# Kernel tuning notes

Hardware: AMD Instinct MI355X
Metric: run time of the kernel (lower is better)

## Reference

```python
import jax, jax.numpy as jnp
import numpy as np

N, D, GN, UVW = 64, 32, 128, 64
EMB = H = 256
NONSP, SPA = 8, 2
ACT = NONSP + 4          # 12
GOA = 256 + ACT          # fc3 + action = 268
GLO = H + GOA            # 524
SW = 64


def _conv3(x, w, b):
    # 3x3, stride 1, pad 1, NCHW / OIHW (torch layout)
    y = jax.lax.conv_general_dilated(x, w, (1, 1), ((1, 1), (1, 1)),
                                     dimension_numbers=('NCHW', 'OIHW', 'NCHW'))
    return y + b[None, :, None, None]


def _up2(x):
    # bilinear x2, half-pixel centers (matches torch align_corners=False)
    n, c, h, w = x.shape
    return jax.image.resize(x, (n, c, 2 * h, 2 * w), 'bilinear')


def setup_inputs() -> dict:
    key = jax.random.key(0)
    ks = jax.random.split(key, 24)
    def rn(k, shape, s=0.05):
        return jax.random.normal(k, shape, jnp.float32) * s
    G = (jax.random.uniform(ks[0], (N, D, GN, GN)) < 0.1).astype(jnp.float32)
    avail = jax.random.randint(ks[2], (N, NONSP), 0, 2).astype(jnp.int32)
    avail = avail.at[:, 0].set(1)  # guarantee at least one available action
    return {
        'G': G,
        'X': rn(ks[1], (N, D, GN, UVW), 1.0),
        'avail_actions': avail,
        'LSTM_hidden': jnp.zeros((2, 1, N, H), jnp.float32),
        'prev_actions': rn(ks[3], (N, D, ACT), 1.0),
        'relevant_frames': jax.random.randint(ks[4], (N, D), 0, 2).astype(jnp.int32),
        'We': rn(ks[5], (UVW, EMB)), 'be': jnp.zeros((EMB,)),
        'W1': rn(ks[6], (EMB, 256)), 'b1': jnp.zeros((256,)),
        'W2': rn(ks[7], (256, 256)), 'b2': jnp.zeros((256,)),
        'W3': rn(ks[8], (256, 256)), 'b3': jnp.zeros((256,)),
        'Wle': rn(ks[9], (GOA, H)), 'ble': jnp.zeros((H,)),
        'Wih': rn(ks[10], (4 * H, H)), 'Whh': rn(ks[11], (4 * H, H)),
        'bih': jnp.zeros((4 * H,)), 'bhh': jnp.zeros((4 * H,)),
        'Wa': rn(ks[12], (GLO, NONSP)), 'ba': jnp.zeros((NONSP,)),
        'Wv': rn(ks[13], (GLO, 1)), 'bv': jnp.zeros((1,)),
        'Wt1': rn(ks[14], (GLO, 256, 4, 4)), 'bt1': jnp.zeros((256,)),
        'Wc2': rn(ks[15], (128, 256, 3, 3)), 'bc2': jnp.zeros((128,)),
        'Wc3': rn(ks[16], (64, 128, 3, 3)), 'bc3': jnp.zeros((64,)),
        'Wc4': rn(ks[17], (64, 64, 3, 3)), 'bc4': jnp.zeros((64,)),
        'Wc5': rn(ks[18], (64, 64, 3, 3)), 'bc5': jnp.zeros((64,)),
        'Wc6': rn(ks[19], (SPA, 64, 3, 3)), 'bc6': jnp.zeros((SPA,)),
    }


def reference(G, X, avail_actions, LSTM_hidden, prev_actions, relevant_frames,
              We, be, W1, b1, W2, b2, W3, b3, Wle, ble, Wih, Whh, bih, bhh,
              Wa, ba, Wv, bv, Wt1, bt1, Wc2, bc2, Wc3, bc3, Wc4, bc4,
              Wc5, bc5, Wc6, bc6):
    n = G.shape[0]
    eye = jnp.eye(GN, dtype=G.dtype)

    def step(carry, xs):
        h, c, _, _ = carry
        Gc, Xc, pa, rel = xs            # [n,GN,GN], [n,GN,UVW], [n,ACT], [n]
        A = Gc + eye
        dis = 1.0 / jnp.sqrt(jnp.maximum(A.sum(-1), 1.0))
        A_agg = A * dis[:, :, None] * dis[:, None, :]  # D^-1/2 A D^-1/2
        emb = jnp.tanh(Xc @ We + be)
        h1 = jnp.tanh(A_agg @ (emb @ W1 + b1))
        h2 = jnp.tanh(A_agg @ (h1 @ W2 + b2))
        h3 = jnp.tanh(A_agg @ (h2 @ W3 + b3))
        goa = jnp.concatenate([h3.max(axis=1), pa], axis=1)  # [n, GOA]
        xin = jnp.tanh(goa @ Wle + ble)
        gates = xin @ Wih.T + bih + h @ Whh.T + bhh
        i, f, g, o = jnp.split(gates, 4, axis=1)
        c_new = jax.nn.sigmoid(f) * c + jax.nn.sigmoid(i) * jnp.tanh(g)
        h_new = jax.nn.sigmoid(o) * jnp.tanh(c_new)
        keep = (rel != 0).astype(h_new.dtype)[:, None]  # reset hidden for irrelevant frames
        return (h_new * keep, c_new * keep, h_new, goa), None

    h0, c0 = LSTM_hidden[0, 0], LSTM_hidden[1, 0]
    goa0 = jnp.zeros((n, GOA), G.dtype)
    xs = (jnp.swapaxes(G, 0, 1), jnp.swapaxes(X, 0, 1),
          jnp.swapaxes(prev_actions, 0, 1), jnp.swapaxes(relevant_frames, 0, 1))
    (hf, cf, hout, goa), _ = jax.lax.scan(step, (h0, c0, h0, goa0), xs)

    glo = jnp.concatenate([hout, goa], axis=1)  # [n, 524]
    logits = glo @ Wa + ba
    logits = jnp.where(avail_actions == 0, -jnp.inf, logits)
    nonspatial_policy = jax.nn.softmax(logits, axis=1)
    value = glo @ Wv + bv

    # deconv on 1x1 input == einsum with torch [in,out,kh,kw] weight
    s1 = jax.nn.leaky_relu(jnp.einsum('nc,cfhw->nfhw', glo, Wt1) + bt1[None, :, None, None], 0.1)
    # note: original F.relu(x, 0.1) is plain relu (0.1 lands in `inplace`)
    s2 = jax.nn.relu(_up2(_conv3(s1, Wc2, bc2)))
    s3 = jax.nn.relu(_up2(_conv3(s2, Wc3, bc3)))
    s4 = jax.nn.relu(_up2(_conv3(s3, Wc4, bc4)))
    s5 = jax.nn.relu(_up2(_conv3(s4, Wc5, bc5)))
    sl = _conv3(s5, Wc6, bc6).reshape(n, SPA, -1)
    spatial_policy = jax.nn.softmax(sl, axis=2).reshape(n, SPA, SW, SW)

    LSTM_hidden_out = jnp.stack([hf, cf])[:, None]  # [2,1,n,H]
    return (spatial_policy, nonspatial_policy, value, LSTM_hidden_out)
```

## Files before the change

### kernel.cpp

```cpp
#include <hip/hip_runtime.h>
#include <math.h>

typedef unsigned short u16;
typedef unsigned int u32;

typedef __attribute__((ext_vector_type(8))) short bf16x8;
typedef __attribute__((ext_vector_type(4))) float f32x4;

__device__ __forceinline__ float b2f(u16 u) {
    union { u32 ui; float f; } v; v.ui = ((u32)u) << 16; return v.f;
}
__device__ __forceinline__ float b2f_lo(u32 u) {
    union { u32 ui; float f; } v; v.ui = u << 16; return v.f;
}
__device__ __forceinline__ float b2f_hi(u32 u) {
    union { u32 ui; float f; } v; v.ui = u & 0xffff0000u; return v.f;
}
__device__ __forceinline__ u16 f2b(float f) {
    union { float f; u32 ui; } v; v.f = f;
    u32 x = v.ui;
    u32 r = (x + 0x7fffu + ((x >> 16) & 1u)) >> 16;
    return (u16)r;
}
__device__ __forceinline__ float sigf(float x) { return 1.0f / (1.0f + expf(-x)); }
__device__ __forceinline__ float ftanh(float x) {
    float e = __expf(2.0f * x);
    return 1.0f - 2.0f / (e + 1.0f);
}

#define GNODES 128
#define EMBD   256
#define NB     64
#define TS     32
#define GOA    268
#define GLO    524

#define OUT_SPATIAL 0
#define OUT_NS      524288
#define OUT_V       524800
#define OUT_H       524864

#define WS_GOA   ((size_t)0)
#define WS_HBUF  ((size_t)2195456)
#define WS_CBUF  ((size_t)2260992)
#define WS_HOUT  ((size_t)2326528)
#define WS_GLO   ((size_t)2392064)
#define WS_WIHT  ((size_t)2526208)
#define WS_WHHT  ((size_t)3574784)
#define WS_BSUM  ((size_t)4623360)
#define WS_C2    ((size_t)4627456)
#define WS_C3    ((size_t)4889600)
#define WS_C4    ((size_t)5413888)
#define WS_C5    ((size_t)7511040)
#define WS_SL    ((size_t)15899648)
#define WS_WET   ((size_t)16948224)
#define WS_W1T   ((size_t)16980992)
#define WS_W2T   ((size_t)17112064)
#define WS_W3T   ((size_t)17243136)
#define WS_GX    ((size_t)17374208)
#define WS_S1F   ((size_t)25762816)

#define WS_WP4   WS_GOA
#define WS_WP5   (WS_GOA + (size_t)196608)
#define WS_WP3   (WS_GOA + (size_t)393216)
#define WS_WP2   WS_GX

#define SA_S 264
#define TT_S 136
#define XS_S 72

__global__ void wprep(const float* __restrict__ We, const float* __restrict__ W1,
                      const float* __restrict__ W2, const float* __restrict__ W3,
                      u16* __restrict__ WeT, u16* __restrict__ W1T,
                      u16* __restrict__ W2T, u16* __restrict__ W3T)
{
    int idx = blockIdx.x * 256 + threadIdx.x;
    if (idx < 16384) {
        int k = idx >> 8, nn = idx & 255;
        WeT[nn * 64 + k] = f2b(We[idx]);
    }
    {
        int k = idx >> 8, nn = idx & 255;
        W1T[nn * 256 + k] = f2b(W1[idx]);
        W2T[nn * 256 + k] = f2b(W2[idx]);
        W3T[nn * 256 + k] = f2b(W3[idx]);
    }
}

__global__ __launch_bounds__(1024, 4) void gcn_mfma(
    const float* __restrict__ G, const float* __restrict__ X, const float* __restrict__ pa,
    const u16* __restrict__ WeT, const float* __restrict__ be,
    const u16* __restrict__ W1T, const float* __restrict__ b1,
    const u16* __restrict__ W2T, const float* __restrict__ b2,
    const u16* __restrict__ W3T, const float* __restrict__ b3,
    float* __restrict__ goaAll)
{
    __shared__ u16 Sa[128 * SA_S];
    __shared__ u16 Tt[256 * TT_S];
    __shared__ float dis[GNODES];
    __shared__ float dred[1024];
    __shared__ float pm[256];

    const int item = blockIdx.x;
    const int tid  = threadIdx.x;
    const int wv   = tid >> 6;
    const int nt   = wv & 7;
    const int ch   = wv >> 3;
    const int lane = tid & 63;
    const int l16  = lane & 15;
    const int quad = lane >> 4;
    const float* Gp = G + (size_t)item * GNODES * GNODES;
    const float* Xp = X + (size_t)item * GNODES * 64;

    for (int idx = tid; idx < 128 * 64; idx += 1024) {
        int m = idx >> 6, k = idx & 63;
        Tt[m * XS_S + k] = f2b(Xp[idx]);
    }
    {
        int row = tid >> 3, part = tid & 7;
        const float4* gr = (const float4*)(Gp + (size_t)row * GNODES) + part * 4;
        float s = 0.f;
#pragma unroll
        for (int k = 0; k < 4; ++k) { float4 g = gr[k]; s += g.x + g.y + g.z + g.w; }
        dred[tid] = s;
    }
    __syncthreads();
    if (tid < GNODES) {
        float s = 0.f;
#pragma unroll
        for (int p = 0; p < 8; ++p) s += dred[tid * 8 + p];
        dis[tid] = 1.0f / sqrtf(s + 1.0f);
    }
    __syncthreads();

    bf16x8 bAgg[4];
    {
        const int i = nt * 16 + l16;
        const float di = dis[i];
        const float* gr = Gp + (size_t)i * GNODES;
#pragma unroll
        for (int t = 0; t < 4; ++t) {
            const int k0 = t * 32 + quad * 8;
            float4 ga = *(const float4*)(gr + k0);
            float4 gb = *(const float4*)(gr + k0 + 4);
            float vv[8] = {ga.x, ga.y, ga.z, ga.w, gb.x, gb.y, gb.z, gb.w};
            bf16x8 f;
#pragma unroll
            for (int j = 0; j < 8; ++j) {
                int k = k0 + j;
                float a = (vv[j] + (k == i ? 1.0f : 0.0f)) * di * dis[k];
                f[j] = (short)f2b(a);
            }
            bAgg[t] = f;
        }
    }

    {
        bf16x8 a0 = *(const bf16x8*)(Tt + (16 * nt + l16) * XS_S + quad * 8);
        bf16x8 a1 = *(const bf16x8*)(Tt + (16 * nt + l16) * XS_S + 32 + quad * 8);
        for (int cj = 0; cj < 8; ++cj) {
            const int ct = ch * 8 + cj;
            const int nf = ct * 16 + l16;
            bf16x8 wb0 = *(const bf16x8*)(WeT + nf * 64 + quad * 8);
            bf16x8 wb1 = *(const bf16x8*)(WeT + nf * 64 + 32 + quad * 8);
            float bb = be[nf];
            f32x4 acc = {bb, bb, bb, bb};
            acc = __builtin_amdgcn_mfma_f32_16x16x32_bf16(a0, wb0, acc, 0, 0, 0);
            acc = __builtin_amdgcn_mfma_f32_16x16x32_bf16(a1, wb1, acc, 0, 0, 0);
#pragma unroll
            for (int r = 0; r < 4; ++r) {
                int node = 16 * nt + quad * 4 + r;
                Sa[node * SA_S + nf] = f2b(ftanh(acc[r]));
            }
        }
    }
    __syncthreads();

    const u16* WTs[3]  = {W1T, W2T, W3T};
    const float* bss[3] = {b1, b2, b3};

    for (int l = 0; l < 3; ++l) {
        const u16* WT = WTs[l];
        const float* bias = bss[l];

        const int nf = wv * 16 + l16;
        const float bb = bias[nf];
        bf16x8 bfr[8];
#pragma unroll
        for (int t = 0; t < 8; ++t)
            bfr[t] = *(const bf16x8*)(WT + (size_t)nf * 256 + t * 32 + quad * 8);

        for (int rt = 0; rt < 8; ++rt) {
            bf16x8 afr[8];
#pragma unroll
            for (int t = 0; t < 8; ++t)
                afr[t] = *(const bf16x8*)(Sa + (16 * rt + l16) * SA_S + t * 32 + quad * 8);
            f32x4 acc = {bb, bb, bb, bb};
#pragma unroll
            for (int t = 0; t < 8; ++t)
                acc = __builtin_amdgcn_mfma_f32_16x16x32_bf16(afr[t], bfr[t], acc, 0, 0, 0);
            u16 p0 = f2b(acc[0]), p1 = f2b(acc[1]), p2 = f2b(acc[2]), p3 = f2b(acc[3]);
            uint2 pk; pk.x = (u32)p0 | ((u32)p1 << 16); pk.y = (u32)p2 | ((u32)p3 << 16);
            *(uint2*)(Tt + (size_t)nf * TT_S + 16 * rt + quad * 4) = pk;
        }
        __syncthreads();

        for (int fj = 0; fj < 8; ++fj) {
            const int ft = ch * 8 + fj;
            bf16x8 afr[4];
#pragma unroll
            for (int t = 0; t < 4; ++t)
                afr[t] = *(const bf16x8*)(Tt + (16 * ft + l16) * TT_S + t * 32 + quad * 8);
            f32x4 acc = {0.f, 0.f, 0.f, 0.f};
#pragma unroll
            for (int t = 0; t < 4; ++t)
                acc = __builtin_amdgcn_mfma_f32_16x16x32_bf16(afr[t], bAgg[t], acc, 0, 0, 0);
            int i = nt * 16 + l16;
            u16 p0 = f2b(ftanh(acc[0])), p1 = f2b(ftanh(acc[1]));
            u16 p2 = f2b(ftanh(acc[2])), p3 = f2b(ftanh(acc[3]));
            uint2 pk; pk.x = (u32)p0 | ((u32)p1 << 16); pk.y = (u32)p2 | ((u32)p3 << 16);
            *(uint2*)(Sa + (size_t)i * SA_S + 16 * ft + quad * 4) = pk;
        }
        __syncthreads();
    }

    const int nb = item >> 5, tt = item & 31;
    float* gdst = goaAll + ((size_t)tt * NB + nb) * GOA;
    float mymax = -2.0f;
    if (tid < 512) {
        int f = tid & 255, h = tid >> 8;
        for (int i = h * 64; i < h * 64 + 64; ++i)
            mymax = fmaxf(mymax, b2f(Sa[i * SA_S + f]));
        if (h == 1) pm[f] = mymax;
    }
    __syncthreads();
    if (tid < 256) {
        gdst[tid] = fmaxf(mymax, pm[tid]);
    } else if (tid >= 512 && tid < 524) {
        gdst[256 + (tid - 512)] = pa[(size_t)item * 12 + (tid - 512)];
    }
}

__global__ void wtrans(const float* __restrict__ Wih, const float* __restrict__ Whh,
                       const float* __restrict__ bih, const float* __restrict__ bhh,
                       float* __restrict__ wihT, float* __restrict__ whhT, float* __restrict__ bsum)
{
    int idx = blockIdx.x * 256 + threadIdx.x;
    int r = idx >> 8;
    int k = idx & 255;
    wihT[k * 1024 + r] = Wih[idx];
    whhT[k * 1024 + r] = Whh[idx];
    if (idx < 1024) bsum[idx] = bih[idx] + bhh[idx];
}

#define LP_IT 8
__global__ __launch_bounds__(256) void lstm_pre(
    const float* __restrict__ goaAll, const float* __restrict__ Wle, const float* __restrict__ ble,
    const float* __restrict__ wihT, const float* __restrict__ bsum,
    float* __restrict__ gatesX)
{
    __shared__ float gl[LP_IT][GOA];
    __shared__ float xv[LP_IT][256];
    const int b0 = blockIdx.x * LP_IT;
    const int u = threadIdx.x;

    for (int idx = u; idx < LP_IT * GOA; idx += 256) {
        int it = idx / GOA, k = idx - it * GOA;
        gl[it][k] = goaAll[(size_t)(b0 + it) * GOA + k];
    }
    __syncthreads();

    {
        float acc[LP_IT];
        float bl = ble[u];
#pragma unroll
        for (int i = 0; i < LP_IT; ++i) acc[i] = bl;
        for (int k = 0; k < GOA; ++k) {
            float w = Wle[k * 256 + u];
#pragma unroll
            for (int i = 0; i < LP_IT; ++i) acc[i] = fmaf(gl[i][k], w, acc[i]);
        }
#pragma unroll
        for (int i = 0; i < LP_IT; ++i) xv[i][u] = tanhf(acc[i]);
    }
    __syncthreads();

#pragma unroll
    for (int g = 0; g < 4; ++g) {
        float a[LP_IT];
        float bs = bsum[g * 256 + u];
#pragma unroll
        for (int i = 0; i < LP_IT; ++i) a[i] = bs;
#pragma unroll 4
        for (int k = 0; k < 256; ++k) {
            float w = wihT[k * 1024 + g * 256 + u];
#pragma unroll
            for (int i = 0; i < LP_IT; ++i) a[i] = fmaf(xv[i][k], w, a[i]);
        }
#pragma unroll
        for (int i = 0; i < LP_IT; ++i)
            gatesX[(size_t)(b0 + i) * 1024 + g * 256 + u] = a[i];
    }
}

__global__ __launch_bounds__(1024) void lstm_seq(
    const float* __restrict__ gatesX, const float* __restrict__ whhT,
    const int* __restrict__ relf, const float* __restrict__ lh,
    float* __restrict__ hbuf, float* __restrict__ cbuf, float* __restrict__ hout)
{
    __shared__ float hv[256];
    __shared__ float ga[1024];
    __shared__ int hzf;
    const int n = blockIdx.x, u = threadIdx.x;
    float cpriv = 0.f;
    if (u < 256) { hv[u] = lh[n * 256 + u]; cpriv = lh[16384 + n * 256 + u]; }
    if (u == 0) hzf = 0;
    __syncthreads();

    for (int t = 0; t < TS; ++t) {
        float a = gatesX[((size_t)t * NB + n) * 1024 + u];
        if (!hzf) {
            const float* wh = whhT + u;
            float a0 = 0.f, a1 = 0.f, a2 = 0.f, a3 = 0.f;
#pragma unroll 4
            for (int k = 0; k < 256; k += 4) {
                a0 = fmaf(hv[k],     wh[(k)     * 1024], a0);
                a1 = fmaf(hv[k + 1], wh[(k + 1) * 1024], a1);
                a2 = fmaf(hv[k + 2], wh[(k + 2) * 1024], a2);
                a3 = fmaf(hv[k + 3], wh[(k + 3) * 1024], a3);
            }
            a += (a0 + a1) + (a2 + a3);
        }
        ga[u] = a;
        __syncthreads();
        if (u < 256) {
            float ai = ga[u], af = ga[256 + u], ag = ga[512 + u], ao = ga[768 + u];
            float cn = sigf(af) * cpriv + sigf(ai) * tanhf(ag);
            float hn = sigf(ao) * tanhf(cn);
            float kp = (relf[n * TS + t] != 0) ? 1.f : 0.f;
            if (t == TS - 1) {
                hout[n * 256 + u] = hn;
                hbuf[n * 256 + u] = hn * kp;
                cbuf[n * 256 + u] = cn * kp;
            }
            cpriv = cn * kp;
            hv[u] = hn * kp;
        }
        if (u == 0) hzf = (relf[n * TS + t] != 0) ? 0 : 1;
        __syncthreads();
    }
}

__global__ __launch_bounds__(256) void heads(
    const float* __restrict__ goaAll, const float* __restrict__ hout,
    const float* __restrict__ hbuf, const float* __restrict__ cbuf,
    const float* __restrict__ Wa, const float* __restrict__ ba,
    const float* __restrict__ Wv, const float* __restrict__ bv,
    const int* __restrict__ avail, float* __restrict__ glo, float* __restrict__ out)
{
    __shared__ float gl[GLO];
    __shared__ float lg[8];
    const int n = blockIdx.x, tid = threadIdx.x;
    const float* gsrc = goaAll + ((size_t)31 * NB + n) * GOA;
    gl[tid] = hout[n * 256 + tid];
    gl[256 + tid] = gsrc[tid];
    if (tid < 12) gl[512 + tid] = gsrc[256 + tid];
    __syncthreads();

    glo[n * GLO + tid]       = gl[tid];
    glo[n * GLO + 256 + tid] = gl[256 + tid];
    if (tid < 12) glo[n * GLO + 512 + tid] = gl[512 + tid];

    out[OUT_H + n * 256 + tid]         = hbuf[n * 256 + tid];
    out[OUT_H + 16384 + n * 256 + tid] = cbuf[n * 256 + tid];

    if (tid < 8) {
        float a = ba[tid];
        for (int k = 0; k < GLO; ++k) a = fmaf(gl[k], Wa[k * 8 + tid], a);
        lg[tid] = (avail[n * 8 + tid] == 0) ? -INFINITY : a;
    } else if (tid == 8) {
        float a = bv[0];
        for (int k = 0; k < GLO; ++k) a = fmaf(gl[k], Wv[k], a);
        out[OUT_V + n] = a;
    }
    __syncthreads();
    if (tid == 0) {
        float m = -INFINITY;
        for (int a = 0; a < 8; ++a) m = fmaxf(m, lg[a]);
        float e[8], s = 0.f;
        for (int a = 0; a < 8; ++a) { e[a] = expf(lg[a] - m); s += e[a]; }
        float inv = 1.f / s;
        for (int a = 0; a < 8; ++a) out[OUT_NS + n * 8 + a] = e[a] * inv;
    }
}

__global__ void wpad_k(const float* __restrict__ Wc4, const float* __restrict__ Wc5,
                       const float* __restrict__ Wc3, const float* __restrict__ Wc2,
                       float* __restrict__ wp4, float* __restrict__ wp5,
                       float* __restrict__ wp3, float* __restrict__ wp2)
{
    int idx = blockIdx.x * 256 + threadIdx.x;
    const float* src; float* dst; int r;
    if (idx < 36864)        { src = Wc4; dst = wp4; r = idx; }
    else if (idx < 73728)   { src = Wc5; dst = wp5; r = idx - 36864; }
    else if (idx < 147456)  { src = Wc3; dst = wp3; r = idx - 73728; }
    else                    { src = Wc2; dst = wp2; r = idx - 147456; }
    int pair = r / 9, q = r - pair * 9;
    dst[pair * 12 + q] = src[r];
}

__global__ __launch_bounds__(256) void deconv1_k(
    const float* __restrict__ glo, const float* __restrict__ Wt1, const float* __restrict__ bt1,
    float* __restrict__ s1f)
{
    const int f = blockIdx.x;
    const int tid = threadIdx.x;
    const int n = tid >> 2, pp = tid & 3;
    float bb = bt1[f];
    float a0 = bb, a1 = bb, a2 = bb, a3 = bb;
    const float* gp = glo + n * GLO;
    for (int c = 0; c < GLO; ++c) {
        float g = gp[c];
        float4 w4 = *(const float4*)&Wt1[(((size_t)c * 256 + f) << 4) + pp * 4];
        a0 = fmaf(g, w4.x, a0);
        a1 = fmaf(g, w4.y, a1);
        a2 = fmaf(g, w4.z, a2);
        a3 = fmaf(g, w4.w, a3);
    }
    float* dst = s1f + (((size_t)n * 256 + f) << 4) + pp * 4;
    dst[0] = a0 > 0.f ? a0 : 0.1f * a0;
    dst[1] = a1 > 0.f ? a1 : 0.1f * a1;
    dst[2] = a2 > 0.f ? a2 : 0.1f * a2;
    dst[3] = a3 > 0.f ? a3 : 0.1f * a3;
}

__global__ __launch_bounds__(256) void conv2_k(
    const float* __restrict__ s1f, const float* __restrict__ wp2, const float* __restrict__ bc2,
    u16* __restrict__ c2)
{
    __shared__ float sp[256 * 36];
    const int n = blockIdx.x >> 3, cot = blockIdx.x & 7;
    const int tid = threadIdx.x;
    for (int i = tid; i < 256 * 36; i += 256) sp[i] = 0.f;
    __syncthreads();
    for (int i = tid; i < 4096; i += 256) {
        int ci = i >> 4, p = i & 15, y = p >> 2, x = p & 3;
        sp[ci * 36 + (y + 1) * 6 + (x + 1)] = s1f[((size_t)n * 256 + ci) * 16 + p];
    }
    __syncthreads();

    const int co = cot * 16 + (tid >> 4);
    const int p = tid & 15, y = p >> 2, x = p & 3;
    float acc = bc2[co];
    const float* wpb = wp2 + (size_t)co * 256 * 12;
    for (int ci = 0; ci < 256; ++ci) {
        const float4* wv4 = (const float4*)(wpb + ci * 12);
        float4 w0 = wv4[0], w1 = wv4[1], w2 = wv4[2];
        float wc[9] = {w0.x, w0.y, w0.z, w0.w, w1.x, w1.y, w1.z, w1.w, w2.x};
        const float* s = sp + ci * 36 + y * 6 + x;
#pragma unroll
        for (int ky = 0; ky < 3; ++ky) {
#pragma unroll
            for (int kx = 0; kx < 3; ++kx)
                acc = fmaf(s[ky * 6 + kx], wc[ky * 3 + kx], acc);
        }
    }
    c2[((size_t)n * 128 + co) * 16 + p] = f2b(acc);
}

template<int CIN, int HI, int WI, int BH, int DW, int COT, int CO>
__global__ __launch_bounds__(256) void up_conv_b(
    const u16* __restrict__ in, const float* __restrict__ wpad, const float* __restrict__ bias,
    u16* __restrict__ out)
{
    constexpr int H2 = 2 * HI, W2 = 2 * WI;
    constexpr int XG = W2 / DW;
    constexpr int ROWS = BH + 2;
    constexpr int STR = W2 + 2;
    constexpr int NBAND = H2 / BH;
    constexpr int CT = CO / COT;
    constexpr int PAIRS = COT / 2;
    static_assert(XG * BH * PAIRS == 256, "thread map must cover block");
    static_assert((STR & 1) == 0, "u32 LDS reads need even u16 stride");

    __shared__ u16 S[CIN * ROWS * STR];

    const int tid = threadIdx.x;
    int b = blockIdx.x;
    const int ct = b % CT; b /= CT;
    const int band = b % NBAND;
    const int n = b / NBAND;
    const int r0 = band * BH;

    const u16* ip = in + (size_t)n * CIN * HI * WI;

    for (int i = tid; i < CIN * ROWS * STR; i += 256) {
        int x  = i % STR;
        int ry = (i / STR) % ROWS;
        int ci = i / (STR * ROWS);
        int yy = r0 - 1 + ry;
        int xx = x - 1;
        float v = 0.f;
        if (yy >= 0 && yy < H2 && xx >= 0 && xx < W2) {
            int y0 = (yy - 1) >> 1; float fy = (yy & 1) ? 0.25f : 0.75f;
            int x0 = (xx - 1) >> 1; float fx = (xx & 1) ? 0.25f : 0.75f;
            int y0c = y0 < 0 ? 0 : y0, y1c = y0 + 1 > HI - 1 ? HI - 1 : y0 + 1;
            int x0c = x0 < 0 ? 0 : x0, x1c = x0 + 1 > WI - 1 ? WI - 1 : x0 + 1;
            const u16* bp = ip + ci * HI * WI;
            float v00 = b2f(bp[y0c * WI + x0c]), v01 = b2f(bp[y0c * WI + x1c]);
            float v10 = b2f(bp[y1c * WI + x0c]), v11 = b2f(bp[y1c * WI + x1c]);
            v = (1.f - fy) * ((1.f - fx) * v00 + fx * v01)
              +        fy  * ((1.f - fx) * v10 + fx * v11);
            v = fmaxf(v, 0.f);
        }
        S[i] = f2b(v);
    }
    __syncthreads();

    const int xg = tid % XG;
    const int y  = (tid / XG) % BH;
    const int pr = tid / (XG * BH);
    const int co0 = ct * COT + pr * 2;
    const int x0 = xg * DW;
    const int yo = r0 + y;

    float acc0[DW], acc1[DW];
    const float bb0 = bias[co0], bb1 = bias[co0 + 1];
#pragma unroll
    for (int d = 0; d < DW; ++d) { acc0[d] = bb0; acc1[d] = bb1; }

    const float* wp0 = wpad + (size_t)(co0 * CIN) * 12;
    const float* wp1 = wpad + (size_t)((co0 + 1) * CIN) * 12;

    for (int ci = 0; ci < CIN; ++ci) {
        float wa[9], wb[9];
        {
            const float4* av = (const float4*)(wp0 + ci * 12);
            float4 a0 = av[0], a1 = av[1], a2 = av[2];
            wa[0] = a0.x; wa[1] = a0.y; wa[2] = a0.z; wa[3] = a0.w;
            wa[4] = a1.x; wa[5] = a1.y; wa[6] = a1.z; wa[7] = a1.w; wa[8] = a2.x;
            const float4* bv = (const float4*)(wp1 + ci * 12);
            float4 b0 = bv[0], b1 = bv[1], b2v = bv[2];
            wb[0] = b0.x; wb[1] = b0.y; wb[2] = b0.z; wb[3] = b0.w;
            wb[4] = b1.x; wb[5] = b1.y; wb[6] = b1.z; wb[7] = b1.w; wb[8] = b2v.x;
        }
#pragma unroll
        for (int ky = 0; ky < 3; ++ky) {
            const u32* Sr = (const u32*)(S + ci * ROWS * STR + (y + ky) * STR + x0);
            float seg[DW + 2];
#pragma unroll
            for (int k = 0; k < (DW + 2) / 2; ++k) {
                u32 u = Sr[k];
                seg[2 * k]     = b2f_lo(u);
                seg[2 * k + 1] = b2f_hi(u);
            }
#pragma unroll
            for (int d = 0; d < DW; ++d) {
                acc0[d] = fmaf(seg[d],     wa[ky * 3 + 0], acc0[d]);
                acc0[d] = fmaf(seg[d + 1], wa[ky * 3 + 1], acc0[d]);
                acc0[d] = fmaf(seg[d + 2], wa[ky * 3 + 2], acc0[d]);
                acc1[d] = fmaf(seg[d],     wb[ky * 3 + 0], acc1[d]);
                acc1[d] = fmaf(seg[d + 1], wb[ky * 3 + 1], acc1[d]);
                acc1[d] = fmaf(seg[d + 2], wb[ky * 3 + 2], acc1[d]);
            }
        }
    }

    u16* op0 = out + (((size_t)(n * CO + co0) * H2) + yo) * W2 + x0;
    u16* op1 = op0 + (size_t)H2 * W2;
#pragma unroll
    for (int d = 0; d < DW; d += 2) {
        u32 p0 = (u32)f2b(acc0[d]) | ((u32)f2b(acc0[d + 1]) << 16);
        u32 p1 = (u32)f2b(acc1[d]) | ((u32)f2b(acc1[d + 1]) << 16);
        *(u32*)(op0 + d) = p0;
        *(u32*)(op1 + d) = p1;
    }
}

__global__ __launch_bounds__(256) void up_conv6(
    const u16* __restrict__ c5, const float* __restrict__ w, const float* __restrict__ bias,
    u16* __restrict__ sl)
{
    __shared__ u16 S[40960];
    const int tid = threadIdx.x;
    const int n = blockIdx.x >> 3;
    const int band = blockIdx.x & 7;
    const int r0 = band * 8;
    const u16* ip = c5 + (size_t)n * 64 * 1024;

    for (int i = tid; i < 40960; i += 256) {
        int x2 = i & 63; int ry = (i >> 6) % 10; int ci = i / 640;
        int yy = r0 - 1 + ry;
        float v = 0.f;
        if (yy >= 0 && yy < 64) {
            int y0 = (yy - 1) >> 1; float fy = (yy & 1) ? 0.25f : 0.75f;
            int x0 = (x2 - 1) >> 1; float fx = (x2 & 1) ? 0.25f : 0.75f;
            int y0c = y0 < 0 ? 0 : y0, y1c = y0 + 1 > 31 ? 31 : y0 + 1;
            int x0c = x0 < 0 ? 0 : x0, x1c = x0 + 1 > 31 ? 31 : x0 + 1;
            const u16* b = ip + ci * 1024;
            float v00 = b2f(b[y0c * 32 + x0c]), v01 = b2f(b[y0c * 32 + x1c]);
            float v10 = b2f(b[y1c * 32 + x0c]), v11 = b2f(b[y1c * 32 + x1c]);
            v = fmaxf((1.f - fy) * ((1.f - fx) * v00 + fx * v01)
                      +      fy  * ((1.f - fx) * v10 + fx * v11), 0.f);
        }
        S[i] = f2b(v);
    }
    __syncthreads();

    {
        const int u = tid;
        const int x0p = (u & 15) * 4;
        const int yr  = (u >> 4) & 7;
        const int co  = u >> 7;
        const int y = r0 + yr;
        float acc[4];
        float bb = bias[co];
#pragma unroll
        for (int d = 0; d < 4; ++d) acc[d] = bb;
        const float* wp = w + (size_t)co * 64 * 9;
        for (int ci = 0; ci < 64; ++ci) {
            const u16* Sr = S + ci * 640;
            float wk[9];
#pragma unroll
            for (int q = 0; q < 9; ++q) wk[q] = wp[ci * 9 + q];
#pragma unroll
            for (int ky = 0; ky < 3; ++ky) {
                int ry = yr + ky;
                float seg[6];
#pragma unroll
                for (int dx = 0; dx < 6; ++dx) {
                    int xx = x0p + dx - 1;
                    seg[dx] = (xx >= 0 && xx < 64) ? b2f(Sr[ry * 64 + xx]) : 0.f;
                }
#pragma unroll
                for (int d = 0; d < 4; ++d) {
                    acc[d] = fmaf(seg[d],     wk[ky * 3 + 0], acc[d]);
                    acc[d] = fmaf(seg[d + 1], wk[ky * 3 + 1], acc[d]);
                    acc[d] = fmaf(seg[d + 2], wk[ky * 3 + 2], acc[d]);
                }
            }
        }
        u16* op = sl + (size_t)(n * 2 + co) * 4096 + y * 64 + x0p;
        u32 p0 = (u32)f2b(acc[0]) | ((u32)f2b(acc[1]) << 16);
        u32 p1 = (u32)f2b(acc[2]) | ((u32)f2b(acc[3]) << 16);
        *(u32*)(op)     = p0;
        *(u32*)(op + 2) = p1;
    }
}

__global__ __launch_bounds__(256) void softmax_spatial(const u16* __restrict__ sl, float* __restrict__ out)
{
    __shared__ float red[256];
    const int b = blockIdx.x;
    const u16* src = sl + (size_t)b * 4096;
    float* dst = out + (size_t)b * 4096;
    const int tid = threadIdx.x;
    float m = -INFINITY;
    for (int i = tid; i < 4096; i += 256) m = fmaxf(m, b2f(src[i]));
    red[tid] = m; __syncthreads();
    for (int s = 128; s > 0; s >>= 1) { if (tid < s) red[tid] = fmaxf(red[tid], red[tid + s]); __syncthreads(); }
    m = red[0]; __syncthreads();
    float sum = 0.f;
    for (int i = tid; i < 4096; i += 256) sum += expf(b2f(src[i]) - m);
    red[tid] = sum; __syncthreads();
    for (int s = 128; s > 0; s >>= 1) { if (tid < s) red[tid] += red[tid + s]; __syncthreads(); }
    float inv = 1.f / red[0];
    for (int i = tid; i < 4096; i += 256) dst[i] = expf(b2f(src[i]) - m) * inv;
}

extern "C" void kernel_launch(void* const* d_in, const int* in_sizes, int n_in,
                              void* d_out, int out_size, void* d_ws, size_t ws_size,
                              hipStream_t stream)
{
    const float* G     = (const float*)d_in[0];
    const float* X     = (const float*)d_in[1];
    const int*   avail = (const int*)d_in[2];
    const float* lh    = (const float*)d_in[3];
    const float* pa    = (const float*)d_in[4];
    const int*   relf  = (const int*)d_in[5];
    const float* We  = (const float*)d_in[6];   const float* be  = (const float*)d_in[7];
    const float* W1  = (const float*)d_in[8];   const float* b1  = (const float*)d_in[9];
    const float* W2  = (const float*)d_in[10];  const float* b2  = (const float*)d_in[11];
    const float* W3  = (const float*)d_in[12];  const float* b3  = (const float*)d_in[13];
    const float* Wle = (const float*)d_in[14];  const float* ble = (const float*)d_in[15];
    const float* Wih = (const float*)d_in[16];  const float* Whh = (const float*)d_in[17];
    const float* bih = (const float*)d_in[18];  const float* bhh = (const float*)d_in[19];
    const float* Wa  = (const float*)d_in[20];  const float* ba  = (const float*)d_in[21];
    const float* Wv  = (const float*)d_in[22];  const float* bv  = (const float*)d_in[23];
    const float* Wt1 = (const float*)d_in[24];  const float* bt1 = (const float*)d_in[25];
    const float* Wc2 = (const float*)d_in[26];  const float* bc2 = (const float*)d_in[27];
    const float* Wc3 = (const float*)d_in[28];  const float* bc3 = (const float*)d_in[29];
    const float* Wc4 = (const float*)d_in[30];  const float* bc4 = (const float*)d_in[31];
    const float* Wc5 = (const float*)d_in[32];  const float* bc5 = (const float*)d_in[33];
    const float* Wc6 = (const float*)d_in[34];  const float* bc6 = (const float*)d_in[35];

    char* ws = (char*)d_ws;
    float* goaAll = (float*)(ws + WS_GOA);
    float* hbuf   = (float*)(ws + WS_HBUF);
    float* cbuf   = (float*)(ws + WS_CBUF);
    float* hout   = (float*)(ws + WS_HOUT);
    float* glo    = (float*)(ws + WS_GLO);
    float* wihT   = (float*)(ws + WS_WIHT);
    float* whhT   = (float*)(ws + WS_WHHT);
    float* bsum   = (float*)(ws + WS_BSUM);
    u16*   c2     = (u16*)(ws + WS_C2);
    u16*   c3     = (u16*)(ws + WS_C3);
    u16*   c4     = (u16*)(ws + WS_C4);
    u16*   c5     = (u16*)(ws + WS_C5);
    u16*   sl     = (u16*)(ws + WS_SL);
    u16*   WeT    = (u16*)(ws + WS_WET);
    u16*   W1T    = (u16*)(ws + WS_W1T);
    u16*   W2T    = (u16*)(ws + WS_W2T);
    u16*   W3T    = (u16*)(ws + WS_W3T);
    float* gatesX = (float*)(ws + WS_GX);
    float* s1f    = (float*)(ws + WS_S1F);
    float* wp4    = (float*)(ws + WS_WP4);
    float* wp5    = (float*)(ws + WS_WP5);
    float* wp3    = (float*)(ws + WS_WP3);
    float* wp2    = (float*)(ws + WS_WP2);
    float* out    = (float*)d_out;

    wprep<<<256, 256, 0, stream>>>(We, W1, W2, W3, WeT, W1T, W2T, W3T);
    wtrans<<<1024, 256, 0, stream>>>(Wih, Whh, bih, bhh, wihT, whhT, bsum);
    gcn_mfma<<<2048, 1024, 0, stream>>>(G, X, pa, WeT, be, W1T, b1, W2T, b2, W3T, b3, goaAll);
    lstm_pre<<<256, 256, 0, stream>>>(goaAll, Wle, ble, wihT, bsum, gatesX);
    lstm_seq<<<64, 1024, 0, stream>>>(gatesX, whhT, relf, lh, hbuf, cbuf, hout);
    heads<<<64, 256, 0, stream>>>(goaAll, hout, hbuf, cbuf, Wa, ba, Wv, bv, avail, glo, out);
    wpad_k<<<1728, 256, 0, stream>>>(Wc4, Wc5, Wc3, Wc2, wp4, wp5, wp3, wp2);
    deconv1_k<<<256, 256, 0, stream>>>(glo, Wt1, bt1, s1f);
    conv2_k<<<512, 256, 0, stream>>>(s1f, wp2, bc2, c2);
    up_conv_b<128, 4, 4, 8, 4, 32, 64><<<128, 256, 0, stream>>>(c2, wp3, bc3, c3);
    up_conv_b<64, 8, 8, 4, 4, 32, 64><<<512, 256, 0, stream>>>(c3, wp4, bc4, c4);
    up_conv_b<64, 16, 16, 4, 8, 32, 64><<<1024, 256, 0, stream>>>(c4, wp5, bc5, c5);
    up_conv6<<<512, 256, 0, stream>>>(c5, Wc6, bc6, sl);
    softmax_spatial<<<128, 256, 0, stream>>>(sl, out + OUT_SPATIAL);
}
```

Baseline: 1.401 ms.

## Repack LSTM recurrent weights as float4 and rebalance lstm_pre and deconv1 work

The recurrent weight matrix is stored interleaved in groups of four k values, so the sequential LSTM step loads one float4 per thread per group instead of four strided scalar loads, cutting load instructions on the serial critical path. lstm_pre now processes 4 items per block over twice as many blocks, with transposed shared buffers read as float4 and all four gates accumulated in one pass over k. deconv1 uses 512 threads with 2 outputs each to raise parallelism. The cost is more register pressure in lstm_pre (16 accumulators) and fewer outputs per thread to hide latency in deconv1.

```diff
diff --git a/kernel.cpp b/kernel.cpp
--- a/kernel.cpp
+++ b/kernel.cpp
@@ -243,30 +243,30 @@
 
 __global__ void wtrans(const float* __restrict__ Wih, const float* __restrict__ Whh,
                        const float* __restrict__ bih, const float* __restrict__ bhh,
-                       float* __restrict__ wihT, float* __restrict__ whhT, float* __restrict__ bsum)
+                       float* __restrict__ wihT, float* __restrict__ whh4, float* __restrict__ bsum)
 {
     int idx = blockIdx.x * 256 + threadIdx.x;
     int r = idx >> 8;
     int k = idx & 255;
     wihT[k * 1024 + r] = Wih[idx];
-    whhT[k * 1024 + r] = Whh[idx];
+    whh4[(size_t)(k >> 2) * 4096 + r * 4 + (k & 3)] = Whh[idx];
     if (idx < 1024) bsum[idx] = bih[idx] + bhh[idx];
 }
 
-#define LP_IT 8
+#define LP_IT 4
 __global__ __launch_bounds__(256) void lstm_pre(
     const float* __restrict__ goaAll, const float* __restrict__ Wle, const float* __restrict__ ble,
     const float* __restrict__ wihT, const float* __restrict__ bsum,
     float* __restrict__ gatesX)
 {
-    __shared__ float gl[LP_IT][GOA];
-    __shared__ float xv[LP_IT][256];
+    __shared__ float glT[GOA * LP_IT];
+    __shared__ float xvT[256 * LP_IT];
     const int b0 = blockIdx.x * LP_IT;
     const int u = threadIdx.x;
 
     for (int idx = u; idx < LP_IT * GOA; idx += 256) {
-        int it = idx / GOA, k = idx - it * GOA;
-        gl[it][k] = goaAll[(size_t)(b0 + it) * GOA + k];
+        int k = idx >> 2, it = idx & 3;
+        glT[idx] = goaAll[(size_t)(b0 + it) * GOA + k];
     }
     __syncthreads();
 
@@ -277,34 +277,52 @@
         for (int i = 0; i < LP_IT; ++i) acc[i] = bl;
         for (int k = 0; k < GOA; ++k) {
             float w = Wle[k * 256 + u];
-#pragma unroll
-            for (int i = 0; i < LP_IT; ++i) acc[i] = fmaf(gl[i][k], w, acc[i]);
-        }
-#pragma unroll
-        for (int i = 0; i < LP_IT; ++i) xv[i][u] = tanhf(acc[i]);
-    }
-    __syncthreads();
-
-#pragma unroll
-    for (int g = 0; g < 4; ++g) {
-        float a[LP_IT];
-        float bs = bsum[g * 256 + u];
-#pragma unroll
-        for (int i = 0; i < LP_IT; ++i) a[i] = bs;
-#pragma unroll 4
+            float4 g4 = *(const float4*)&glT[k * 4];
+            acc[0] = fmaf(g4.x, w, acc[0]);
+            acc[1] = fmaf(g4.y, w, acc[1]);
+            acc[2] = fmaf(g4.z, w, acc[2]);
+            acc[3] = fmaf(g4.w, w, acc[3]);
+        }
+        float4 xv4;
+        xv4.x = tanhf(acc[0]); xv4.y = tanhf(acc[1]);
+        xv4.z = tanhf(acc[2]); xv4.w = tanhf(acc[3]);
+        *(float4*)&xvT[u * 4] = xv4;
+    }
+    __syncthreads();
+
+    {
+        float a[4][LP_IT];
+#pragma unroll
+        for (int g = 0; g < 4; ++g) {
+            float bs = bsum[g * 256 + u];
+#pragma unroll
+            for (int i = 0; i < LP_IT; ++i) a[g][i] = bs;
+        }
         for (int k = 0; k < 256; ++k) {
-            float w = wihT[k * 1024 + g * 256 + u];
-#pragma unroll
-            for (int i = 0; i < LP_IT; ++i) a[i] = fmaf(xv[i][k], w, a[i]);
-        }
-#pragma unroll
-        for (int i = 0; i < LP_IT; ++i)
-            gatesX[(size_t)(b0 + i) * 1024 + g * 256 + u] = a[i];
+            float4 x4 = *(const float4*)&xvT[k * 4];
+            float w0 = wihT[k * 1024 + u];
+            float w1 = wihT[k * 1024 + 256 + u];
+            float w2 = wihT[k * 1024 + 512 + u];
+            float w3 = wihT[k * 1024 + 768 + u];
+            a[0][0] = fmaf(x4.x, w0, a[0][0]); a[0][1] = fmaf(x4.y, w0, a[0][1]);
+            a[0][2] = fmaf(x4.z, w0, a[0][2]); a[0][3] = fmaf(x4.w, w0, a[0][3]);
+            a[1][0] = fmaf(x4.x, w1, a[1][0]); a[1][1] = fmaf(x4.y, w1, a[1][1]);
+            a[1][2] = fmaf(x4.z, w1, a[1][2]); a[1][3] = fmaf(x4.w, w1, a[1][3]);
+            a[2][0] = fmaf(x4.x, w2, a[2][0]); a[2][1] = fmaf(x4.y, w2, a[2][1]);
+            a[2][2] = fmaf(x4.z, w2, a[2][2]); a[2][3] = fmaf(x4.w, w2, a[2][3]);
+            a[3][0] = fmaf(x4.x, w3, a[3][0]); a[3][1] = fmaf(x4.y, w3, a[3][1]);
+            a[3][2] = fmaf(x4.z, w3, a[3][2]); a[3][3] = fmaf(x4.w, w3, a[3][3]);
+        }
+#pragma unroll
+        for (int g = 0; g < 4; ++g)
+#pragma unroll
+            for (int i = 0; i < LP_IT; ++i)
+                gatesX[(size_t)(b0 + i) * 1024 + g * 256 + u] = a[g][i];
     }
 }
 
 __global__ __launch_bounds__(1024) void lstm_seq(
-    const float* __restrict__ gatesX, const float* __restrict__ whhT,
+    const float* __restrict__ gatesX, const float* __restrict__ whh4,
     const int* __restrict__ relf, const float* __restrict__ lh,
     float* __restrict__ hbuf, float* __restrict__ cbuf, float* __restrict__ hout)
 {
@@ -317,17 +335,20 @@
     if (u == 0) hzf = 0;
     __syncthreads();
 
+    const float4* w4base = (const float4*)whh4 + u;
+
     for (int t = 0; t < TS; ++t) {
         float a = gatesX[((size_t)t * NB + n) * 1024 + u];
         if (!hzf) {
-            const float* wh = whhT + u;
             float a0 = 0.f, a1 = 0.f, a2 = 0.f, a3 = 0.f;
 #pragma unroll 4
-            for (int k = 0; k < 256; k += 4) {
-                a0 = fmaf(hv[k],     wh[(k)     * 1024], a0);
-                a1 = fmaf(hv[k + 1], wh[(k + 1) * 1024], a1);
-                a2 = fmaf(hv[k + 2], wh[(k + 2) * 1024], a2);
-                a3 = fmaf(hv[k + 3], wh[(k + 3) * 1024], a3);
+            for (int k4 = 0; k4 < 64; ++k4) {
+                float4 w = w4base[k4 * 1024];
+                int k = k4 * 4;
+                a0 = fmaf(hv[k],     w.x, a0);
+                a1 = fmaf(hv[k + 1], w.y, a1);
+                a2 = fmaf(hv[k + 2], w.z, a2);
+                a3 = fmaf(hv[k + 3], w.w, a3);
             }
             a += (a0 + a1) + (a2 + a3);
         }
@@ -409,29 +430,25 @@
     dst[pair * 12 + q] = src[r];
 }
 
-__global__ __launch_bounds__(256) void deconv1_k(
+__global__ __launch_bounds__(512) void deconv1_k(
     const float* __restrict__ glo, const float* __restrict__ Wt1, const float* __restrict__ bt1,
     float* __restrict__ s1f)
 {
     const int f = blockIdx.x;
     const int tid = threadIdx.x;
-    const int n = tid >> 2, pp = tid & 3;
+    const int n = tid >> 3, pp = tid & 7;
     float bb = bt1[f];
-    float a0 = bb, a1 = bb, a2 = bb, a3 = bb;
+    float a0 = bb, a1 = bb;
     const float* gp = glo + n * GLO;
     for (int c = 0; c < GLO; ++c) {
         float g = gp[c];
-        float4 w4 = *(const float4*)&Wt1[(((size_t)c * 256 + f) << 4) + pp * 4];
-        a0 = fmaf(g, w4.x, a0);
-        a1 = fmaf(g, w4.y, a1);
-        a2 = fmaf(g, w4.z, a2);
-        a3 = fmaf(g, w4.w, a3);
-    }
-    float* dst = s1f + (((size_t)n * 256 + f) << 4) + pp * 4;
+        float2 w2 = *(const float2*)&Wt1[(((size_t)c * 256 + f) << 4) + pp * 2];
+        a0 = fmaf(g, w2.x, a0);
+        a1 = fmaf(g, w2.y, a1);
+    }
+    float* dst = s1f + (((size_t)n * 256 + f) << 4) + pp * 2;
     dst[0] = a0 > 0.f ? a0 : 0.1f * a0;
     dst[1] = a1 > 0.f ? a1 : 0.1f * a1;
-    dst[2] = a2 > 0.f ? a2 : 0.1f * a2;
-    dst[3] = a3 > 0.f ? a3 : 0.1f * a3;
 }
 
 __global__ __launch_bounds__(256) void conv2_k(
@@ -701,7 +718,7 @@
     float* hout   = (float*)(ws + WS_HOUT);
     float* glo    = (float*)(ws + WS_GLO);
     float* wihT   = (float*)(ws + WS_WIHT);
-    float* whhT   = (float*)(ws + WS_WHHT);
+    float* whh4   = (float*)(ws + WS_WHHT);
     float* bsum   = (float*)(ws + WS_BSUM);
     u16*   c2     = (u16*)(ws + WS_C2);
     u16*   c3     = (u16*)(ws + WS_C3);
@@ -721,13 +738,13 @@
     float* out    = (float*)d_out;
 
     wprep<<<256, 256, 0, stream>>>(We, W1, W2, W3, WeT, W1T, W2T, W3T);
-    wtrans<<<1024, 256, 0, stream>>>(Wih, Whh, bih, bhh, wihT, whhT, bsum);
+    wtrans<<<1024, 256, 0, stream>>>(Wih, Whh, bih, bhh, wihT, whh4, bsum);
     gcn_mfma<<<2048, 1024, 0, stream>>>(G, X, pa, WeT, be, W1T, b1, W2T, b2, W3T, b3, goaAll);
-    lstm_pre<<<256, 256, 0, stream>>>(goaAll, Wle, ble, wihT, bsum, gatesX);
-    lstm_seq<<<64, 1024, 0, stream>>>(gatesX, whhT, relf, lh, hbuf, cbuf, hout);
+    lstm_pre<<<512, 256, 0, stream>>>(goaAll, Wle, ble, wihT, bsum, gatesX);
+    lstm_seq<<<64, 1024, 0, stream>>>(gatesX, whh4, relf, lh, hbuf, cbuf, hout);
     heads<<<64, 256, 0, stream>>>(goaAll, hout, hbuf, cbuf, Wa, ba, Wv, bv, avail, glo, out);
     wpad_k<<<1728, 256, 0, stream>>>(Wc4, Wc5, Wc3, Wc2, wp4, wp5, wp3, wp2);
-    deconv1_k<<<256, 256, 0, stream>>>(glo, Wt1, bt1, s1f);
+    deconv1_k<<<256, 512, 0, stream>>>(glo, Wt1, bt1, s1f);
     conv2_k<<<512, 256, 0, stream>>>(s1f, wp2, bc2, c2);
     up_conv_b<128, 4, 4, 8, 4, 32, 64><<<128, 256, 0, stream>>>(c2, wp3, bc3, c3);
     up_conv_b<64, 8, 8, 4, 4, 32, 64><<<512, 256, 0, stream>>>(c3, wp4, bc4, c4);
```

New measurement: 1.313 ms. 1.07x faster.
